# Kernel optimization log

Measured on AMD Instinct MI355X. Metric: run time of the kernel, lower is better.

The kernel has to match this reference:

```python
import jax, jax.numpy as jnp
import numpy as np

N, M, DIST, HEADS, D, C, DFFN = 16384, 16, 2, 8, 256, 64, 512
DH = D // HEADS
GRID = 128
BLOCK = 2048  # mirrors torch batch_size loop in find_neighboring_voxels_optimized
EPS = 1e-5


def _neighbors(coords_f, src, m, dist):
    """Blockwise Manhattan-distance topk neighbor gather.
    coords_f: (N,3) float voxel coords; src: (N,D) features.
    Returns (N, m, D) neighbor features, zero-filled where fewer than m in range."""
    n = coords_f.shape[0]
    qblocks = coords_f.reshape(-1, BLOCK, 3)

    def one_block(cb):
        # (BLOCK, N) Manhattan distances
        d = jnp.abs(cb[:, None, :] - coords_f[None, :, :]).sum(-1)
        d = jnp.where(d <= dist, d, jnp.inf)
        vals, idx = jax.lax.top_k(-d, m)          # nearest m (self first: dist 0)
        valid = (vals > -jnp.inf)[..., None]
        return jnp.where(valid, src[idx], jnp.zeros((), src.dtype))

    return jax.lax.map(one_block, qblocks).reshape(n, m, src.shape[-1])


def _layernorm(x, g, b):
    mu = x.mean(-1, keepdims=True)
    var = ((x - mu) ** 2).mean(-1, keepdims=True)
    return (x - mu) * jax.lax.rsqrt(var + EPS) * g + b


def setup_inputs() -> dict:
    key = jax.random.key(0)
    ks = jax.random.split(key, 32)
    p = lambda i, shape, s: jax.random.normal(ks[i], shape, dtype=jnp.float32) * s
    z = lambda shape: jnp.zeros(shape, dtype=jnp.float32)
    o = lambda shape: jnp.ones(shape, dtype=jnp.float32)
    return {
        "coords": jax.random.randint(ks[0], (N, 3), 0, GRID, dtype=jnp.int32),
        "features": jax.random.normal(ks[1], (N, C), dtype=jnp.float32),
        "pe_w1": p(2, (3, D // 2), 0.5), "pe_b1": z((D // 2,)),
        "pe_w2": p(3, (D // 2, D), 0.08), "pe_b2": z((D,)),
        "proj_w": p(4, (C, D), 0.12), "proj_b": z((D,)),
        "wq": p(5, (D, D), 0.06), "bq": z((D,)),
        "wk": p(6, (D, D), 0.06), "bk": z((D,)),
        "wv": p(7, (D, D), 0.06), "bv": z((D,)),
        "wo": p(8, (D, D), 0.06), "bo": z((D,)),
        "ffn_w1": p(9, (D, DFFN), 0.06), "ffn_b1": z((DFFN,)),
        "ffn_w2": p(10, (DFFN, D), 0.04), "ffn_b2": z((D,)),
        "ln_g": o((D,)), "ln_b": z((D,)),
        "fus_w1": p(11, (D, C), 0.06), "fus_b1": z((C,)),
        "fus_w2": p(12, (2 * C, C), 0.09), "fus_b2": z((C,)),
        "bn_g": o((C,)), "bn_b": z((C,)),
    }


def reference(coords, features, pe_w1, pe_b1, pe_w2, pe_b2, proj_w, proj_b,
              wq, bq, wk, bk, wv, bv, wo, bo,
              ffn_w1, ffn_b1, ffn_w2, ffn_b2, ln_g, ln_b,
              fus_w1, fus_b1, fus_w2, fus_b2, bn_g, bn_b):
    coords_f = coords.astype(jnp.float32)
    # dynamic learnable positional encoding on normalized coords
    xn = coords_f / (GRID - 1)
    pe = jax.nn.relu(xn @ pe_w1 + pe_b1) @ pe_w2 + pe_b2
    src = features @ proj_w + proj_b + pe                       # (N, D)

    nf = _neighbors(coords_f, src, M, DIST)                     # (N, M, D)
    query = nf[:, 0, :]                                         # (N, D) self-feature

    # multihead attention: query len 1, key len M, batch N
    q = (query @ wq + bq).reshape(N, HEADS, DH)
    k = (nf @ wk + bk).reshape(N, M, HEADS, DH)
    v = (nf @ wv + bv).reshape(N, M, HEADS, DH)
    scores = jnp.einsum('nhd,nmhd->nhm', q, k) / jnp.sqrt(jnp.float32(DH))
    attn = jax.nn.softmax(scores, axis=-1)
    ao = jnp.einsum('nhm,nmhd->nhd', attn, v).reshape(N, D) @ wo + bo  # (N, D)

    # FFN with residual + LayerNorm (dropout=0 / eval)
    h = jax.nn.relu(ao @ ffn_w1 + ffn_b1) @ ffn_w2 + ffn_b2
    y = _layernorm(ao + h, ln_g, ln_b)                          # (N, D)

    # EnhancedFusion: project, concat, linear, BatchNorm1d (batch stats), ReLU
    t = y @ fus_w1 + fus_b1                                     # (N, C)
    f = jnp.concatenate([features, t], axis=1) @ fus_w2 + fus_b2
    mu = f.mean(0)
    var = ((f - mu) ** 2).mean(0)
    f = (f - mu) * jax.lax.rsqrt(var + EPS) * bn_g + bn_b
    return jax.nn.relu(f)                                       # (N, C)
```

## Files before the change

kernel.cpp:

```cpp
#include <hip/hip_runtime.h>
#include <stdint.h>

typedef unsigned short u16;
typedef unsigned int   u32;
typedef __attribute__((ext_vector_type(8))) short short8;
typedef __attribute__((ext_vector_type(4))) float f32x4;

static constexpr int kN = 16384;
static constexpr float kEPS = 1e-5f;

__device__ __forceinline__ u16 f2bf(float x) {
  u32 u = __float_as_uint(x);
  u32 r = (u + 0x7fffu + ((u >> 16) & 1u)) >> 16;
  return (u16)r;
}
__device__ __forceinline__ float bf2f(u16 x) {
  return __uint_as_float(((u32)x) << 16);
}
__device__ __forceinline__ void ldbf8(const u16* p, float* o) {
  uint4 v = *(const uint4*)p;
  o[0] = __uint_as_float(v.x << 16);  o[1] = __uint_as_float(v.x & 0xffff0000u);
  o[2] = __uint_as_float(v.y << 16);  o[3] = __uint_as_float(v.y & 0xffff0000u);
  o[4] = __uint_as_float(v.z << 16);  o[5] = __uint_as_float(v.z & 0xffff0000u);
  o[6] = __uint_as_float(v.w << 16);  o[7] = __uint_as_float(v.w & 0xffff0000u);
}
__device__ __forceinline__ void gll16(const u16* g, u16* l) {
  __builtin_amdgcn_global_load_lds(
      (const __attribute__((address_space(1))) void*)g,
      (__attribute__((address_space(3))) void*)l, 16, 0, 0);
}

struct WSet {
  const float* s[6]; u16* d[6];
  int K[6]; int N[6]; int dstride[6]; int coff[6];
};

__global__ __launch_bounds__(256) void k_setup(WSet ws,
                                               u32* __restrict__ zero_area,
                                               const float* __restrict__ proj_b,
                                               const float* __restrict__ pe_b2,
                                               const float* __restrict__ uw1,
                                               const float* __restrict__ ub1,
                                               const float* __restrict__ uw2,
                                               const float* __restrict__ ub2,
                                               u16* __restrict__ W2f,
                                               float* __restrict__ bbf,
                                               const int* __restrict__ coords,
                                               const float* __restrict__ feats,
                                               const float* __restrict__ pw1,
                                               const float* __restrict__ pb1,
                                               u16* __restrict__ A1,
                                               u16* __restrict__ A2,
                                               const float* __restrict__ wq,
                                               const float* __restrict__ wk,
                                               const float* __restrict__ wv,
                                               const float* __restrict__ proj_w_f,
                                               const float* __restrict__ pe_w2_f,
                                               u16* __restrict__ W1K,
                                               float* __restrict__ bcomb) {
  int w = blockIdx.y;
  if (w == 6) {
    int idx = blockIdx.x * 256 + threadIdx.x;
    if (idx < 33088) zero_area[idx] = 0u;
    return;
  }
  if (w == 7) {
    int n = blockIdx.x;
    if (n >= 64) return;
    int k = threadIdx.x;
    float s = 0.f;
    for (int j = 0; j < 64; j++) s += uw1[k * 64 + j] * uw2[(64 + j) * 64 + n];
    W2f[n * 320 + k] = f2bf(s);
    if (k < 64) W2f[n * 320 + 256 + k] = f2bf(uw2[k * 64 + n]);
    if (k == 0) {
      float b = ub2[n];
      for (int j = 0; j < 64; j++) b += ub1[j] * uw2[(64 + j) * 64 + n];
      bbf[n] = b;
    }
    return;
  }
  if (w == 8) {
    int r0 = blockIdx.x * 32;
#pragma unroll
    for (int s = 0; s < 3; s++) {
      int j = threadIdx.x + s * 256;
      int row = j / 24, seg = j % 24;
      int n = r0 + row;
      u16 o[8];
      if (seg < 8) {
        const float* fp = feats + (size_t)n * 64 + seg * 8;
        float4 a = *(const float4*)fp;
        float4 b = *(const float4*)(fp + 4);
        o[0] = f2bf(a.x); o[1] = f2bf(a.y); o[2] = f2bf(a.z); o[3] = f2bf(a.w);
        o[4] = f2bf(b.x); o[5] = f2bf(b.y); o[6] = f2bf(b.z); o[7] = f2bf(b.w);
        *(uint4*)(A2 + (size_t)n * 320 + 256 + seg * 8) = *(uint4*)o;
      } else {
        int jj0 = (seg - 8) * 8;
        float x0 = (float)coords[n * 3 + 0] * (1.f / 127.f);
        float x1 = (float)coords[n * 3 + 1] * (1.f / 127.f);
        float x2 = (float)coords[n * 3 + 2] * (1.f / 127.f);
#pragma unroll
        for (int u = 0; u < 8; u++) {
          int jj = jj0 + u;
          float hv = pb1[jj] + x0 * pw1[jj] + x1 * pw1[128 + jj] + x2 * pw1[256 + jj];
          o[u] = f2bf(fmaxf(hv, 0.f));
        }
      }
      *(uint4*)(A1 + (size_t)n * 192 + seg * 8) = *(uint4*)o;
    }
    return;
  }
  if (w == 9) {
    int bx = blockIdx.x;
    if (bx < 3) {
      const float* wsel = (bx == 0) ? wq : (bx == 1) ? wk : wv;
      int c = threadIdx.x;
      float s = 0.f;
      for (int d = 0; d < 256; d++) s += (proj_b[d] + pe_b2[d]) * wsel[d * 256 + c];
      bcomb[bx * 256 + c] = s;
    } else if (bx < 27) {
      int i0 = (bx - 3) * 2048 + threadIdx.x * 8;
      const float* src = (i0 < 16384) ? (proj_w_f + i0) : (pe_w2_f + (i0 - 16384));
      float4 a = *(const float4*)src;
      float4 b = *(const float4*)(src + 4);
      u16 o[8];
      o[0] = f2bf(a.x); o[1] = f2bf(a.y); o[2] = f2bf(a.z); o[3] = f2bf(a.w);
      o[4] = f2bf(b.x); o[5] = f2bf(b.y); o[6] = f2bf(b.z); o[7] = f2bf(b.w);
      *(uint4*)(W1K + i0) = *(uint4*)o;
    }
    return;
  }
  const float* S = ws.s[w]; u16* D = ws.d[w];
  int K = ws.K[w], N = ws.N[w], ds = ws.dstride[w], co = ws.coff[w];
  int ntx = N >> 5, tiles = ntx * (K >> 5);
  int t = blockIdx.x;
  if (t >= tiles) return;
  int n0 = (t % ntx) * 32, k0 = (t / ntx) * 32;
  __shared__ float st[32][33];
  int tr = threadIdx.x >> 3, tc4 = (threadIdx.x & 7) * 4;
  float4 v = *(const float4*)(S + (size_t)(k0 + tr) * N + n0 + tc4);
  st[tc4 + 0][tr] = v.x; st[tc4 + 1][tr] = v.y;
  st[tc4 + 2][tr] = v.z; st[tc4 + 3][tr] = v.w;
  __syncthreads();
  u16 o4[4];
  o4[0] = f2bf(st[tr][tc4 + 0]); o4[1] = f2bf(st[tr][tc4 + 1]);
  o4[2] = f2bf(st[tr][tc4 + 2]); o4[3] = f2bf(st[tr][tc4 + 3]);
  *(uint2*)(D + (size_t)(n0 + tr) * ds + co + k0 + tc4) = *(uint2*)o4;
}


__global__ __launch_bounds__(256) void k_hist(const int* __restrict__ coords,
                                              u32* __restrict__ cnt) {
  int n = blockIdx.x * 256 + threadIdx.x;
  int c = coords[n * 3] * 128 + coords[n * 3 + 1];
  atomicAdd(&cnt[c], 1u);
}

__global__ __launch_bounds__(256) void k_scan(const u32* __restrict__ cnt,
                                              u32* __restrict__ startb) {
  __shared__ u32 tots[256];
  int t = threadIdx.x;
  int base = t * 64;
  u32 s = 0;
  for (int i = 0; i < 64; i++) s += cnt[base + i];
  tots[t] = s;
  __syncthreads();
  if (t == 0) {
    u32 run = 0;
    for (int i = 0; i < 256; i++) { u32 v = tots[i]; tots[i] = run; run += v; }
  }
  __syncthreads();
  u32 run = tots[t];
  for (int i = 0; i < 64; i++) { startb[base + i] = run; run += cnt[base + i]; }
}

__global__ __launch_bounds__(256) void k_scatter(const int* __restrict__ coords,
                                                 const u32* __restrict__ startb,
                                                 u32* __restrict__ cursor,
                                                 u32* __restrict__ pts) {
  int n = blockIdx.x * 256 + threadIdx.x;
  int x = coords[n * 3], y = coords[n * 3 + 1], z = coords[n * 3 + 2];
  int c = x * 128 + y;
  u32 slot = atomicAdd(&cursor[c], 1u);
  pts[startb[c] + slot] = ((u32)z << 14) | (u32)n;
}

__global__ __launch_bounds__(256) void k_select(const int* __restrict__ coords,
                                                const u32* __restrict__ startb,
                                                const u32* __restrict__ cnt,
                                                const u32* __restrict__ pts,
                                                int* __restrict__ idxo) {
  int n = blockIdx.x * 256 + threadIdx.x;
  int x = coords[n * 3], y = coords[n * 3 + 1], z = coords[n * 3 + 2];
  u32 best[16];
#pragma unroll
  for (int j = 0; j < 16; j++) best[j] = 0xFFFFFFFFu;
  const int dxs[13] = {0, -1, 1, 0, 0, -2, 2, 0, 0, -1, -1, 1, 1};
  const int dys[13] = {0, 0, 0, -1, 1, 0, 0, -2, 2, -1, 1, -1, 1};
  const int dbs[13] = {0, 1, 1, 1, 1, 2, 2, 2, 2, 2, 2, 2, 2};
#pragma unroll
  for (int t = 0; t < 13; t++) {
    int xx = x + dxs[t], yy = y + dys[t];
    if (xx < 0 || xx > 127 || yy < 0 || yy > 127) continue;
    int c = xx * 128 + yy;
    u32 s0 = startb[c], e0 = s0 + cnt[c];
    for (u32 i = s0; i < e0; ++i) {
      u32 p = pts[i];
      int zq = (int)(p >> 14);
      int id = (int)(p & 16383u);
      int az = z - zq; az = az < 0 ? -az : az;
      int dd = dbs[t] + az;
      u32 key = (dd <= 2) ? (((u32)dd << 14) | (u32)id) : 0xFFFFFFFFu;
#pragma unroll
      for (int j = 0; j < 16; j++) {
        u32 lo = min(best[j], key);
        u32 hi = max(best[j], key);
        best[j] = lo; key = hi;
      }
    }
  }
#pragma unroll
  for (int j = 0; j < 16; j++)
    idxo[n * 16 + j] = (best[j] == 0xFFFFFFFFu) ? -1 : (int)(best[j] & 16383u);
}

template <int BM, int BN, int ACT, int OUTBF, int ADD>
__global__ __launch_bounds__(256) void k_mgemm(
    const u16* __restrict__ A, const u16* __restrict__ WT,
    const float* __restrict__ bias,
    void* __restrict__ Cout,
    const u16* __restrict__ Addp,
    int M, int K, int N) {
  constexpr int FM = BM / 32, FN = BN / 32;
  constexpr int RA = BM / 64, RB = BN / 64;
  __shared__ __align__(16) u16 As[2][BM * 32];
  __shared__ __align__(16) u16 Bs[2][BN * 32];
  const int tid = threadIdx.x;
  const int wave = tid >> 6, lane = tid & 63;
  const int bm = blockIdx.y * BM, bn = blockIdx.x * BN;
  const int wr = (wave >> 1) * (BM / 2), wc = (wave & 1) * (BN / 2);
  const int fr = lane & 15, fk = (lane >> 4) * 8, rq = (lane >> 4) * 4;

  f32x4 acc[FM][FN];
#pragma unroll
  for (int i = 0; i < FM; i++)
#pragma unroll
    for (int j = 0; j < FN; j++)
#pragma unroll
      for (int r = 0; r < 4; r++) acc[i][j][r] = 0.f;

  for (int k0 = 0; k0 < K; k0 += 64) {
#pragma unroll
    for (int h = 0; h < 2; h++) {
#pragma unroll
      for (int r = 0; r < RA; r++) {
        int g2 = r * 256 + tid;
        gll16(A + (size_t)(bm + (g2 >> 2)) * K + k0 + h * 32 + (g2 & 3) * 8,
              As[h] + g2 * 8);
      }
#pragma unroll
      for (int r = 0; r < RB; r++) {
        int g2 = r * 256 + tid;
        gll16(WT + (size_t)(bn + (g2 >> 2)) * K + k0 + h * 32 + (g2 & 3) * 8,
              Bs[h] + g2 * 8);
      }
    }
    __syncthreads();
#pragma unroll
    for (int h = 0; h < 2; h++) {
      short8 af[FM], bg[FN];
#pragma unroll
      for (int i = 0; i < FM; i++)
        af[i] = *(const short8*)&As[h][(wr + i * 16 + fr) * 32 + fk];
#pragma unroll
      for (int j = 0; j < FN; j++)
        bg[j] = *(const short8*)&Bs[h][(wc + j * 16 + fr) * 32 + fk];
#pragma unroll
      for (int i = 0; i < FM; i++)
#pragma unroll
        for (int j = 0; j < FN; j++)
          acc[i][j] = __builtin_amdgcn_mfma_f32_16x16x32_bf16(af[i], bg[j], acc[i][j], 0, 0, 0);
    }
    __syncthreads();
  }

#pragma unroll
  for (int j = 0; j < FN; j++) {
    int cc = bn + wc + j * 16 + fr;
    float bval = bias ? bias[cc] : 0.f;
#pragma unroll
    for (int i = 0; i < FM; i++) {
      int rbase = bm + wr + i * 16 + rq;
#pragma unroll
      for (int r = 0; r < 4; r++) {
        float v = acc[i][j][r] + bval;
        size_t o = (size_t)(rbase + r) * N + cc;
        if (ADD) v += bf2f(Addp[o]);
        if (ACT) v = fmaxf(v, 0.f);
        if (OUTBF) ((u16*)Cout)[o] = f2bf(v);
        else       ((float*)Cout)[o] = v;
      }
    }
  }
}

__global__ __launch_bounds__(256) void k_attn(const u16* __restrict__ QKV,
                                              const u32* __restrict__ pts,
                                              const int* __restrict__ idx,
                                              const float* __restrict__ bq,
                                              const float* __restrict__ bk,
                                              const float* __restrict__ bv,
                                              u16* __restrict__ outp) {
  int gid = blockIdx.x * 256 + threadIdx.x;
  int n = (int)(pts[gid >> 3] & 16383u), h = gid & 7;
  const int* ip = idx + n * 16;
  const int hb = h * 32;
  float q[32];
  {
    int i0 = ip[0];
    const u16* qp = QKV + (size_t)i0 * 768 + hb;
#pragma unroll
    for (int j = 0; j < 32; j += 8) ldbf8(qp + j, &q[j]);
#pragma unroll
    for (int j = 0; j < 32; j++) q[j] += bq[hb + j];
  }
  float qbk = 0.f;
#pragma unroll
  for (int j = 0; j < 32; j++) qbk += q[j] * bk[hb + j];
  float s[16]; int ii[16];
#pragma unroll
  for (int m = 0; m < 16; m++) {
    int i = ip[m]; ii[m] = i;
    float d = qbk;
    if (i >= 0) {
      const u16* kp = QKV + (size_t)i * 768 + 256 + hb;
      float kv[32];
#pragma unroll
      for (int j = 0; j < 32; j += 8) ldbf8(kp + j, &kv[j]);
#pragma unroll
      for (int j = 0; j < 32; j++) d += q[j] * kv[j];
    }
    s[m] = d * 0.17677669529663689f;
  }
  float mx = s[0];
#pragma unroll
  for (int m = 1; m < 16; m++) mx = fmaxf(mx, s[m]);
  float sum = 0.f;
#pragma unroll
  for (int m = 0; m < 16; m++) { s[m] = __expf(s[m] - mx); sum += s[m]; }
  float inv = 1.f / sum;
  float o[32];
#pragma unroll
  for (int j = 0; j < 32; j++) o[j] = 0.f;
#pragma unroll
  for (int m = 0; m < 16; m++) {
    if (ii[m] >= 0) {
      const u16* vp = QKV + (size_t)ii[m] * 768 + 512 + hb;
      float vv[32];
#pragma unroll
      for (int j = 0; j < 32; j += 8) ldbf8(vp + j, &vv[j]);
#pragma unroll
      for (int j = 0; j < 32; j++) o[j] += s[m] * vv[j];
    }
  }
  u16* op = outp + (size_t)n * 256 + hb;
#pragma unroll
  for (int j = 0; j < 32; j += 8) {
    u16 tmp[8];
#pragma unroll
    for (int jj = 0; jj < 8; jj++) tmp[jj] = f2bf(o[j + jj] * inv + bv[hb + j + jj]);
    *(uint4*)(op + j) = *(uint4*)tmp;
  }
}

__global__ __launch_bounds__(256) void k_ln(const u16* __restrict__ xx,
                                            const float* __restrict__ g,
                                            const float* __restrict__ b,
                                            u16* __restrict__ A2) {
  int row = blockIdx.x * 4 + (threadIdx.x >> 6);
  int lane = threadIdx.x & 63;
  uint2 raw = *(const uint2*)(xx + (size_t)row * 256 + lane * 4);
  float x0 = __uint_as_float(raw.x << 16), x1 = __uint_as_float(raw.x & 0xffff0000u);
  float x2 = __uint_as_float(raw.y << 16), x3 = __uint_as_float(raw.y & 0xffff0000u);
  float sm = x0 + x1 + x2 + x3;
#pragma unroll
  for (int off = 1; off < 64; off <<= 1) sm += __shfl_xor(sm, off);
  float mu = sm * (1.f / 256.f);
  float d0 = x0 - mu, d1 = x1 - mu, d2 = x2 - mu, d3 = x3 - mu;
  float sq = d0 * d0 + d1 * d1 + d2 * d2 + d3 * d3;
#pragma unroll
  for (int off = 1; off < 64; off <<= 1) sq += __shfl_xor(sq, off);
  float rstd = rsqrtf(sq * (1.f / 256.f) + kEPS);
  float4 gv = *(const float4*)(g + lane * 4);
  float4 bv4 = *(const float4*)(b + lane * 4);
  u16 o[4];
  o[0] = f2bf(d0 * rstd * gv.x + bv4.x); o[1] = f2bf(d1 * rstd * gv.y + bv4.y);
  o[2] = f2bf(d2 * rstd * gv.z + bv4.z); o[3] = f2bf(d3 * rstd * gv.w + bv4.w);
  *(uint2*)(A2 + (size_t)row * 320 + lane * 4) = *(uint2*)o;
}

__global__ __launch_bounds__(256) void k_fgemm(const u16* __restrict__ A2,
                                               const u16* __restrict__ W2f,
                                               const float* __restrict__ bbf,
                                               float* __restrict__ fB,
                                               float* __restrict__ pS,
                                               float* __restrict__ pQ) {
  __shared__ __align__(16) u16 As[2][2048];
  __shared__ __align__(16) u16 Bs[2][2048];
  __shared__ float colS[64][2], colQ[64][2];
  const int tid = threadIdx.x;
  const int wave = tid >> 6, lane = tid & 63;
  const int bm = blockIdx.x * 64;
  const int wr = (wave >> 1) * 32, wc = (wave & 1) * 32;
  const int fr = lane & 15, fk = (lane >> 4) * 8, rq = (lane >> 4) * 4;
  const int g = wave * 64 + lane;
  const int grow = g >> 2, gko = (g & 3) * 8;

  f32x4 acc[2][2];
#pragma unroll
  for (int i = 0; i < 2; i++)
#pragma unroll
    for (int j = 0; j < 2; j++)
#pragma unroll
      for (int r = 0; r < 4; r++) acc[i][j][r] = 0.f;
  for (int k0 = 0; k0 < 320; k0 += 64) {
#pragma unroll
    for (int h = 0; h < 2; h++) {
      gll16(A2 + (size_t)(bm + grow) * 320 + k0 + h * 32 + gko, As[h] + g * 8);
      gll16(W2f + (size_t)grow * 320 + k0 + h * 32 + gko, Bs[h] + g * 8);
    }
    __syncthreads();
#pragma unroll
    for (int h = 0; h < 2; h++) {
      short8 af[2], bg[2];
#pragma unroll
      for (int i = 0; i < 2; i++)
        af[i] = *(const short8*)&As[h][(wr + i * 16 + fr) * 32 + fk];
#pragma unroll
      for (int j = 0; j < 2; j++)
        bg[j] = *(const short8*)&Bs[h][(wc + j * 16 + fr) * 32 + fk];
#pragma unroll
      for (int i = 0; i < 2; i++)
#pragma unroll
        for (int j = 0; j < 2; j++)
          acc[i][j] = __builtin_amdgcn_mfma_f32_16x16x32_bf16(af[i], bg[j], acc[i][j], 0, 0, 0);
    }
    __syncthreads();
  }
  float cS[2] = {0.f, 0.f}, cQ[2] = {0.f, 0.f};
#pragma unroll
  for (int j = 0; j < 2; j++) {
    int col = wc + j * 16 + fr;
    float bv = bbf[col];
#pragma unroll
    for (int i = 0; i < 2; i++) {
      int rbase = bm + wr + i * 16 + rq;
#pragma unroll
      for (int r = 0; r < 4; r++) {
        float v = acc[i][j][r] + bv;
        fB[(size_t)(rbase + r) * 64 + col] = v;
        cS[j] += v; cQ[j] += v * v;
      }
    }
  }
#pragma unroll
  for (int off = 16; off < 64; off <<= 1) {
#pragma unroll
    for (int j = 0; j < 2; j++) {
      cS[j] += __shfl_xor(cS[j], off);
      cQ[j] += __shfl_xor(cQ[j], off);
    }
  }
  if ((lane >> 4) == 0) {
#pragma unroll
    for (int j = 0; j < 2; j++) {
      colS[wc + j * 16 + fr][wave >> 1] = cS[j];
      colQ[wc + j * 16 + fr][wave >> 1] = cQ[j];
    }
  }
  __syncthreads();
  if (tid < 64) {
    atomicAdd(&pS[tid], colS[tid][0] + colS[tid][1]);
    atomicAdd(&pQ[tid], colQ[tid][0] + colQ[tid][1]);
  }
}

__global__ __launch_bounds__(64) void k_bnfin(const float* __restrict__ pS,
                                              const float* __restrict__ pQ,
                                              const float* __restrict__ g,
                                              const float* __restrict__ b,
                                              float* __restrict__ coef,
                                              float* __restrict__ shift) {
  int c = threadIdx.x;
  float S = pS[c], Q = pQ[c];
  float m = S * (1.f / 16384.f);
  float var = Q * (1.f / 16384.f) - m * m;
  float cf = rsqrtf(var + kEPS) * g[c];
  coef[c] = cf;
  shift[c] = b[c] - m * cf;
}

__global__ __launch_bounds__(256) void k_bnapply(const float* __restrict__ f,
                                                 const float* __restrict__ coef,
                                                 const float* __restrict__ shift,
                                                 float* __restrict__ out) {
  int gid = blockIdx.x * 256 + threadIdx.x;
  int e = gid * 4, col = e & 63;
  float4 v = *(const float4*)(f + e);
  float4 cf = *(const float4*)(coef + col);
  float4 sh = *(const float4*)(shift + col);
  float4 o;
  o.x = fmaxf(v.x * cf.x + sh.x, 0.f);
  o.y = fmaxf(v.y * cf.y + sh.y, 0.f);
  o.z = fmaxf(v.z * cf.z + sh.z, 0.f);
  o.w = fmaxf(v.w * cf.w + sh.w, 0.f);
  *(float4*)(out + e) = o;
}

extern "C" void kernel_launch(void* const* d_in, const int* in_sizes, int n_in,
                              void* d_out, int out_size, void* d_ws, size_t ws_size,
                              hipStream_t stream) {
  (void)in_sizes; (void)n_in; (void)out_size; (void)ws_size;
  const int*   coords = (const int*)d_in[0];
  const float* feats  = (const float*)d_in[1];
  const float* pe_w1  = (const float*)d_in[2];
  const float* pe_b1  = (const float*)d_in[3];
  const float* pe_w2  = (const float*)d_in[4];
  const float* pe_b2  = (const float*)d_in[5];
  const float* proj_w = (const float*)d_in[6];
  const float* proj_b = (const float*)d_in[7];
  const float* wq  = (const float*)d_in[8];
  const float* bq  = (const float*)d_in[9];
  const float* wk  = (const float*)d_in[10];
  const float* bk  = (const float*)d_in[11];
  const float* wv  = (const float*)d_in[12];
  const float* bv  = (const float*)d_in[13];
  const float* wo  = (const float*)d_in[14];
  const float* bo  = (const float*)d_in[15];
  const float* fw1 = (const float*)d_in[16];
  const float* fb1 = (const float*)d_in[17];
  const float* fw2 = (const float*)d_in[18];
  const float* fb2 = (const float*)d_in[19];
  const float* lng = (const float*)d_in[20];
  const float* lnb = (const float*)d_in[21];
  const float* uw1 = (const float*)d_in[22];
  const float* ub1 = (const float*)d_in[23];
  const float* uw2 = (const float*)d_in[24];
  const float* ub2 = (const float*)d_in[25];
  const float* bng = (const float*)d_in[26];
  const float* bnb = (const float*)d_in[27];
  float* out = (float*)d_out;

  char* Wc = (char*)d_ws;
  const size_t MB = 1u << 20;
  u16*   A1    = (u16*)(Wc + 0 * MB);
  u16*   QKVb  = (u16*)(Wc + 14 * MB);
  u16*   aoInB = (u16*)(Wc + 38 * MB);
  u16*   aoB   = (u16*)(Wc + 46 * MB);
  u16*   h1B   = (u16*)(Wc + 54 * MB);
  u16*   xBb   = (u16*)(Wc + 70 * MB);
  u16*   A2    = (u16*)(Wc + 78 * MB);
  float* fB    = (float*)(Wc + 0 * MB);

  u16* qkvT  = (u16*)(Wc + 88 * MB);
  u16* woT   = qkvT + 196608;
  u16* fw1T  = woT + 65536;
  u16* fw2T  = fw1T + 131072;
  u16* W1K   = fw2T + 131072;
  u16* W2f   = W1K + 49152;
  u16* Wcomb = W2f + 20480;
  float* bbf   = (float*)(Wcomb + 147456);
  float* bcomb = bbf + 64;

  u32* Z      = (u32*)(Wc + 90 * MB);
  u32* cnt    = Z;
  u32* cursor = Z + 16384;
  float* pS   = (float*)(Z + 32768);
  float* pQ   = (float*)(Z + 32832);
  float* coefb = (float*)(Z + 32912);
  float* shb   = coefb + 64;
  u32* startb = Z + 33280;
  u32* pts    = Z + 49664;
  int* idxb   = (int*)(Z + 66048);

  WSet ws;
  ws.s[0] = wq;     ws.d[0] = qkvT;          ws.K[0] = 256; ws.N[0] = 256; ws.dstride[0] = 256; ws.coff[0] = 0;
  ws.s[1] = wk;     ws.d[1] = qkvT + 65536;  ws.K[1] = 256; ws.N[1] = 256; ws.dstride[1] = 256; ws.coff[1] = 0;
  ws.s[2] = wv;     ws.d[2] = qkvT + 131072; ws.K[2] = 256; ws.N[2] = 256; ws.dstride[2] = 256; ws.coff[2] = 0;
  ws.s[3] = wo;     ws.d[3] = woT;           ws.K[3] = 256; ws.N[3] = 256; ws.dstride[3] = 256; ws.coff[3] = 0;
  ws.s[4] = fw1;    ws.d[4] = fw1T;          ws.K[4] = 256; ws.N[4] = 512; ws.dstride[4] = 256; ws.coff[4] = 0;
  ws.s[5] = fw2;    ws.d[5] = fw2T;          ws.K[5] = 512; ws.N[5] = 256; ws.dstride[5] = 512; ws.coff[5] = 0;

  k_setup<<<dim3(512, 10), 256, 0, stream>>>(ws, Z, proj_b, pe_b2,
                                             uw1, ub1, uw2, ub2, W2f, bbf,
                                             coords, feats, pe_w1, pe_b1, A1, A2,
                                             wq, wk, wv, proj_w, pe_w2, W1K, bcomb);
  k_mgemm<64, 64, 0, 1, 0><<<dim3(3, 12), 256, 0, stream>>>(
      qkvT, W1K, nullptr, Wcomb, nullptr, 768, 256, 192);
  k_hist<<<64, 256, 0, stream>>>(coords, cnt);
  k_scan<<<1, 256, 0, stream>>>(cnt, startb);
  k_scatter<<<64, 256, 0, stream>>>(coords, startb, cursor, pts);
  k_select<<<64, 256, 0, stream>>>(coords, startb, cnt, pts, idxb);
  k_mgemm<128, 128, 0, 1, 0><<<dim3(6, 128), 256, 0, stream>>>(
      A1, Wcomb, bcomb, QKVb, nullptr, kN, 192, 768);
  k_attn<<<512, 256, 0, stream>>>(QKVb, pts, idxb, bq, bk, bv, aoInB);
  k_mgemm<128, 64, 0, 1, 0><<<dim3(4, 128), 256, 0, stream>>>(
      aoInB, woT, bo, aoB, nullptr, kN, 256, 256);
  k_mgemm<128, 128, 1, 1, 0><<<dim3(4, 128), 256, 0, stream>>>(
      aoB, fw1T, fb1, h1B, nullptr, kN, 256, 512);
  k_mgemm<128, 64, 0, 1, 1><<<dim3(4, 128), 256, 0, stream>>>(
      h1B, fw2T, fb2, xBb, aoB, kN, 512, 256);
  k_ln<<<4096, 256, 0, stream>>>(xBb, lng, lnb, A2);
  k_fgemm<<<256, 256, 0, stream>>>(A2, W2f, bbf, fB, pS, pQ);
  k_bnfin<<<1, 64, 0, stream>>>(pS, pQ, bng, bnb, coefb, shb);
  k_bnapply<<<1024, 256, 0, stream>>>(fB, coefb, shb, out);
}
```

Before: 249.4 us.

## Fuse neighbor build, FFN2+LayerNorm, and fusion GEMM+BatchNorm via cooperative grid sync

Merges the histogram/scan/scatter/select kernels into one cooperative kernel that uses grid.sync between phases. Fuses the second FFN GEMM with the residual add and LayerNorm, using a 64x256 tile so each block holds full rows. Fuses the final GEMM with BatchNorm statistics, finalisation and ReLU through a grid-wide barrier, which removes the intermediate fB round trip and three launches. The costs are grid-sync overhead, cooperative-launch limits, lower GEMM parallelism (256 blocks) in the FFN2 stage, and a one-pass variance formula.

```diff
diff --git a/kernel.cpp b/kernel.cpp
--- a/kernel.cpp
+++ b/kernel.cpp
@@ -1,5 +1,8 @@
 #include <hip/hip_runtime.h>
+#include <hip/hip_cooperative_groups.h>
 #include <stdint.h>
+
+namespace cg = cooperative_groups;
 
 typedef unsigned short u16;
 typedef unsigned int   u32;
@@ -148,50 +151,38 @@
   *(uint2*)(D + (size_t)(n0 + tr) * ds + co + k0 + tc4) = *(uint2*)o4;
 }
 
-
-__global__ __launch_bounds__(256) void k_hist(const int* __restrict__ coords,
-                                              u32* __restrict__ cnt) {
-  int n = blockIdx.x * 256 + threadIdx.x;
-  int c = coords[n * 3] * 128 + coords[n * 3 + 1];
-  atomicAdd(&cnt[c], 1u);
-}
-
-__global__ __launch_bounds__(256) void k_scan(const u32* __restrict__ cnt,
-                                              u32* __restrict__ startb) {
-  __shared__ u32 tots[256];
-  int t = threadIdx.x;
-  int base = t * 64;
-  u32 s = 0;
-  for (int i = 0; i < 64; i++) s += cnt[base + i];
-  tots[t] = s;
-  __syncthreads();
-  if (t == 0) {
-    u32 run = 0;
-    for (int i = 0; i < 256; i++) { u32 v = tots[i]; tots[i] = run; run += v; }
-  }
-  __syncthreads();
-  u32 run = tots[t];
-  for (int i = 0; i < 64; i++) { startb[base + i] = run; run += cnt[base + i]; }
-}
-
-__global__ __launch_bounds__(256) void k_scatter(const int* __restrict__ coords,
-                                                 const u32* __restrict__ startb,
-                                                 u32* __restrict__ cursor,
-                                                 u32* __restrict__ pts) {
+__global__ __launch_bounds__(256) void k_neigh(const int* __restrict__ coords,
+                                               u32* __restrict__ cnt,
+                                               u32* __restrict__ startb,
+                                               u32* __restrict__ cursor,
+                                               u32* __restrict__ pts,
+                                               int* __restrict__ idxo) {
+  cg::grid_group grid = cg::this_grid();
   int n = blockIdx.x * 256 + threadIdx.x;
   int x = coords[n * 3], y = coords[n * 3 + 1], z = coords[n * 3 + 2];
   int c = x * 128 + y;
+  atomicAdd(&cnt[c], 1u);
+  grid.sync();
+  if (blockIdx.x == 0) {
+    __shared__ u32 tots[256];
+    int t = threadIdx.x;
+    int base = t * 64;
+    u32 s = 0;
+    for (int i = 0; i < 64; i++) s += cnt[base + i];
+    tots[t] = s;
+    __syncthreads();
+    if (t == 0) {
+      u32 run = 0;
+      for (int i = 0; i < 256; i++) { u32 v = tots[i]; tots[i] = run; run += v; }
+    }
+    __syncthreads();
+    u32 run = tots[t];
+    for (int i = 0; i < 64; i++) { startb[base + i] = run; run += cnt[base + i]; }
+  }
+  grid.sync();
   u32 slot = atomicAdd(&cursor[c], 1u);
   pts[startb[c] + slot] = ((u32)z << 14) | (u32)n;
-}
-
-__global__ __launch_bounds__(256) void k_select(const int* __restrict__ coords,
-                                                const u32* __restrict__ startb,
-                                                const u32* __restrict__ cnt,
-                                                const u32* __restrict__ pts,
-                                                int* __restrict__ idxo) {
-  int n = blockIdx.x * 256 + threadIdx.x;
-  int x = coords[n * 3], y = coords[n * 3 + 1], z = coords[n * 3 + 2];
+  grid.sync();
   u32 best[16];
 #pragma unroll
   for (int j = 0; j < 16; j++) best[j] = 0xFFFFFFFFu;
@@ -202,8 +193,8 @@
   for (int t = 0; t < 13; t++) {
     int xx = x + dxs[t], yy = y + dys[t];
     if (xx < 0 || xx > 127 || yy < 0 || yy > 127) continue;
-    int c = xx * 128 + yy;
-    u32 s0 = startb[c], e0 = s0 + cnt[c];
+    int cc = xx * 128 + yy;
+    u32 s0 = startb[cc], e0 = s0 + cnt[cc];
     for (u32 i = s0; i < e0; ++i) {
       u32 p = pts[i];
       int zq = (int)(p >> 14);
@@ -373,38 +364,127 @@
   }
 }
 
-__global__ __launch_bounds__(256) void k_ln(const u16* __restrict__ xx,
-                                            const float* __restrict__ g,
-                                            const float* __restrict__ b,
-                                            u16* __restrict__ A2) {
-  int row = blockIdx.x * 4 + (threadIdx.x >> 6);
-  int lane = threadIdx.x & 63;
-  uint2 raw = *(const uint2*)(xx + (size_t)row * 256 + lane * 4);
-  float x0 = __uint_as_float(raw.x << 16), x1 = __uint_as_float(raw.x & 0xffff0000u);
-  float x2 = __uint_as_float(raw.y << 16), x3 = __uint_as_float(raw.y & 0xffff0000u);
-  float sm = x0 + x1 + x2 + x3;
-#pragma unroll
-  for (int off = 1; off < 64; off <<= 1) sm += __shfl_xor(sm, off);
-  float mu = sm * (1.f / 256.f);
-  float d0 = x0 - mu, d1 = x1 - mu, d2 = x2 - mu, d3 = x3 - mu;
-  float sq = d0 * d0 + d1 * d1 + d2 * d2 + d3 * d3;
-#pragma unroll
-  for (int off = 1; off < 64; off <<= 1) sq += __shfl_xor(sq, off);
-  float rstd = rsqrtf(sq * (1.f / 256.f) + kEPS);
-  float4 gv = *(const float4*)(g + lane * 4);
-  float4 bv4 = *(const float4*)(b + lane * 4);
-  u16 o[4];
-  o[0] = f2bf(d0 * rstd * gv.x + bv4.x); o[1] = f2bf(d1 * rstd * gv.y + bv4.y);
-  o[2] = f2bf(d2 * rstd * gv.z + bv4.z); o[3] = f2bf(d3 * rstd * gv.w + bv4.w);
-  *(uint2*)(A2 + (size_t)row * 320 + lane * 4) = *(uint2*)o;
-}
-
-__global__ __launch_bounds__(256) void k_fgemm(const u16* __restrict__ A2,
-                                               const u16* __restrict__ W2f,
-                                               const float* __restrict__ bbf,
-                                               float* __restrict__ fB,
-                                               float* __restrict__ pS,
-                                               float* __restrict__ pQ) {
+__global__ __launch_bounds__(256) void k_ffn2ln(const u16* __restrict__ A,
+                                                const u16* __restrict__ WT,
+                                                const float* __restrict__ bias,
+                                                const u16* __restrict__ Addp,
+                                                const float* __restrict__ g,
+                                                const float* __restrict__ b,
+                                                u16* __restrict__ A2) {
+  constexpr int BM = 64, BN = 256, FM = 2, FN = 8;
+  __shared__ __align__(16) u16 As[2][BM * 32];
+  __shared__ __align__(16) u16 Bs[2][BN * 32];
+  __shared__ float lnS[64][2], lnQ[64][2];
+  const int tid = threadIdx.x;
+  const int wave = tid >> 6, lane = tid & 63;
+  const int bm = blockIdx.x * BM;
+  const int wr = (wave >> 1) * 32, wc = (wave & 1) * 128;
+  const int fr = lane & 15, fk = (lane >> 4) * 8, rq = (lane >> 4) * 4;
+
+  f32x4 acc[FM][FN];
+#pragma unroll
+  for (int i = 0; i < FM; i++)
+#pragma unroll
+    for (int j = 0; j < FN; j++)
+#pragma unroll
+      for (int r = 0; r < 4; r++) acc[i][j][r] = 0.f;
+
+  for (int k0 = 0; k0 < 512; k0 += 64) {
+#pragma unroll
+    for (int h = 0; h < 2; h++) {
+      {
+        int g2 = tid;
+        gll16(A + (size_t)(bm + (g2 >> 2)) * 512 + k0 + h * 32 + (g2 & 3) * 8,
+              As[h] + g2 * 8);
+      }
+#pragma unroll
+      for (int r = 0; r < 4; r++) {
+        int g2 = r * 256 + tid;
+        gll16(WT + (size_t)(g2 >> 2) * 512 + k0 + h * 32 + (g2 & 3) * 8,
+              Bs[h] + g2 * 8);
+      }
+    }
+    __syncthreads();
+#pragma unroll
+    for (int h = 0; h < 2; h++) {
+      short8 af[FM], bg[FN];
+#pragma unroll
+      for (int i = 0; i < FM; i++)
+        af[i] = *(const short8*)&As[h][(wr + i * 16 + fr) * 32 + fk];
+#pragma unroll
+      for (int j = 0; j < FN; j++)
+        bg[j] = *(const short8*)&Bs[h][(wc + j * 16 + fr) * 32 + fk];
+#pragma unroll
+      for (int i = 0; i < FM; i++)
+#pragma unroll
+        for (int j = 0; j < FN; j++)
+          acc[i][j] = __builtin_amdgcn_mfma_f32_16x16x32_bf16(af[i], bg[j], acc[i][j], 0, 0, 0);
+    }
+    __syncthreads();
+  }
+
+#pragma unroll
+  for (int j = 0; j < FN; j++) {
+    int cc = wc + j * 16 + fr;
+    float bval = bias[cc];
+#pragma unroll
+    for (int i = 0; i < FM; i++) {
+      int rbase = bm + wr + i * 16 + rq;
+#pragma unroll
+      for (int r = 0; r < 4; r++)
+        acc[i][j][r] += bval + bf2f(Addp[(size_t)(rbase + r) * 256 + cc]);
+    }
+  }
+#pragma unroll
+  for (int i = 0; i < FM; i++) {
+#pragma unroll
+    for (int r = 0; r < 4; r++) {
+      float sm = 0.f, sq = 0.f;
+#pragma unroll
+      for (int j = 0; j < FN; j++) { float t = acc[i][j][r]; sm += t; sq += t * t; }
+#pragma unroll
+      for (int off = 1; off < 16; off <<= 1) {
+        sm += __shfl_xor(sm, off);
+        sq += __shfl_xor(sq, off);
+      }
+      if (fr == 0) {
+        int row = wr + i * 16 + rq + r;
+        lnS[row][wave & 1] = sm;
+        lnQ[row][wave & 1] = sq;
+      }
+    }
+  }
+  __syncthreads();
+#pragma unroll
+  for (int i = 0; i < FM; i++) {
+#pragma unroll
+    for (int r = 0; r < 4; r++) {
+      int row = wr + i * 16 + rq + r;
+      float sm = lnS[row][0] + lnS[row][1];
+      float sq = lnQ[row][0] + lnQ[row][1];
+      float mu = sm * (1.f / 256.f);
+      float var = sq * (1.f / 256.f) - mu * mu;
+      float rstd = rsqrtf(var + kEPS);
+      size_t rowg = (size_t)(bm + row);
+#pragma unroll
+      for (int j = 0; j < FN; j++) {
+        int cc = wc + j * 16 + fr;
+        float val = (acc[i][j][r] - mu) * rstd * g[cc] + b[cc];
+        A2[rowg * 320 + cc] = f2bf(val);
+      }
+    }
+  }
+}
+
+__global__ __launch_bounds__(256) void k_fgemmbn(const u16* __restrict__ A2,
+                                                 const u16* __restrict__ W2f,
+                                                 const float* __restrict__ bbf,
+                                                 float* __restrict__ pS,
+                                                 float* __restrict__ pQ,
+                                                 const float* __restrict__ g,
+                                                 const float* __restrict__ b,
+                                                 float* __restrict__ out) {
+  cg::grid_group grid = cg::this_grid();
   __shared__ __align__(16) u16 As[2][2048];
   __shared__ __align__(16) u16 Bs[2][2048];
   __shared__ float colS[64][2], colQ[64][2];
@@ -413,8 +493,8 @@
   const int bm = blockIdx.x * 64;
   const int wr = (wave >> 1) * 32, wc = (wave & 1) * 32;
   const int fr = lane & 15, fk = (lane >> 4) * 8, rq = (lane >> 4) * 4;
-  const int g = wave * 64 + lane;
-  const int grow = g >> 2, gko = (g & 3) * 8;
+  const int gg = wave * 64 + lane;
+  const int grow = gg >> 2, gko = (gg & 3) * 8;
 
   f32x4 acc[2][2];
 #pragma unroll
@@ -426,8 +506,8 @@
   for (int k0 = 0; k0 < 320; k0 += 64) {
 #pragma unroll
     for (int h = 0; h < 2; h++) {
-      gll16(A2 + (size_t)(bm + grow) * 320 + k0 + h * 32 + gko, As[h] + g * 8);
-      gll16(W2f + (size_t)grow * 320 + k0 + h * 32 + gko, Bs[h] + g * 8);
+      gll16(A2 + (size_t)(bm + grow) * 320 + k0 + h * 32 + gko, As[h] + gg * 8);
+      gll16(W2f + (size_t)grow * 320 + k0 + h * 32 + gko, Bs[h] + gg * 8);
     }
     __syncthreads();
 #pragma unroll
@@ -454,11 +534,10 @@
     float bv = bbf[col];
 #pragma unroll
     for (int i = 0; i < 2; i++) {
-      int rbase = bm + wr + i * 16 + rq;
 #pragma unroll
       for (int r = 0; r < 4; r++) {
         float v = acc[i][j][r] + bv;
-        fB[(size_t)(rbase + r) * 64 + col] = v;
+        acc[i][j][r] = v;
         cS[j] += v; cQ[j] += v * v;
       }
     }
@@ -483,38 +562,23 @@
     atomicAdd(&pS[tid], colS[tid][0] + colS[tid][1]);
     atomicAdd(&pQ[tid], colQ[tid][0] + colQ[tid][1]);
   }
-}
-
-__global__ __launch_bounds__(64) void k_bnfin(const float* __restrict__ pS,
-                                              const float* __restrict__ pQ,
-                                              const float* __restrict__ g,
-                                              const float* __restrict__ b,
-                                              float* __restrict__ coef,
-                                              float* __restrict__ shift) {
-  int c = threadIdx.x;
-  float S = pS[c], Q = pQ[c];
-  float m = S * (1.f / 16384.f);
-  float var = Q * (1.f / 16384.f) - m * m;
-  float cf = rsqrtf(var + kEPS) * g[c];
-  coef[c] = cf;
-  shift[c] = b[c] - m * cf;
-}
-
-__global__ __launch_bounds__(256) void k_bnapply(const float* __restrict__ f,
-                                                 const float* __restrict__ coef,
-                                                 const float* __restrict__ shift,
-                                                 float* __restrict__ out) {
-  int gid = blockIdx.x * 256 + threadIdx.x;
-  int e = gid * 4, col = e & 63;
-  float4 v = *(const float4*)(f + e);
-  float4 cf = *(const float4*)(coef + col);
-  float4 sh = *(const float4*)(shift + col);
-  float4 o;
-  o.x = fmaxf(v.x * cf.x + sh.x, 0.f);
-  o.y = fmaxf(v.y * cf.y + sh.y, 0.f);
-  o.z = fmaxf(v.z * cf.z + sh.z, 0.f);
-  o.w = fmaxf(v.w * cf.w + sh.w, 0.f);
-  *(float4*)(out + e) = o;
+  grid.sync();
+#pragma unroll
+  for (int j = 0; j < 2; j++) {
+    int col = wc + j * 16 + fr;
+    float S = pS[col], Q = pQ[col];
+    float m = S * (1.f / 16384.f);
+    float var = Q * (1.f / 16384.f) - m * m;
+    float cf = rsqrtf(var + kEPS) * g[col];
+    float sh = b[col] - m * cf;
+#pragma unroll
+    for (int i = 0; i < 2; i++) {
+      int rbase = bm + wr + i * 16 + rq;
+#pragma unroll
+      for (int r = 0; r < 4; r++)
+        out[(size_t)(rbase + r) * 64 + col] = fmaxf(acc[i][j][r] * cf + sh, 0.f);
+    }
+  }
 }
 
 extern "C" void kernel_launch(void* const* d_in, const int* in_sizes, int n_in,
@@ -558,9 +622,7 @@
   u16*   aoInB = (u16*)(Wc + 38 * MB);
   u16*   aoB   = (u16*)(Wc + 46 * MB);
   u16*   h1B   = (u16*)(Wc + 54 * MB);
-  u16*   xBb   = (u16*)(Wc + 70 * MB);
   u16*   A2    = (u16*)(Wc + 78 * MB);
-  float* fB    = (float*)(Wc + 0 * MB);
 
   u16* qkvT  = (u16*)(Wc + 88 * MB);
   u16* woT   = qkvT + 196608;
@@ -577,8 +639,6 @@
   u32* cursor = Z + 16384;
   float* pS   = (float*)(Z + 32768);
   float* pQ   = (float*)(Z + 32832);
-  float* coefb = (float*)(Z + 32912);
-  float* shb   = coefb + 64;
   u32* startb = Z + 33280;
   u32* pts    = Z + 49664;
   int* idxb   = (int*)(Z + 66048);
@@ -597,10 +657,11 @@
                                              wq, wk, wv, proj_w, pe_w2, W1K, bcomb);
   k_mgemm<64, 64, 0, 1, 0><<<dim3(3, 12), 256, 0, stream>>>(
       qkvT, W1K, nullptr, Wcomb, nullptr, 768, 256, 192);
-  k_hist<<<64, 256, 0, stream>>>(coords, cnt);
-  k_scan<<<1, 256, 0, stream>>>(cnt, startb);
-  k_scatter<<<64, 256, 0, stream>>>(coords, startb, cursor, pts);
-  k_select<<<64, 256, 0, stream>>>(coords, startb, cnt, pts, idxb);
+  {
+    void* args[] = {(void*)&coords, (void*)&cnt, (void*)&startb,
+                    (void*)&cursor, (void*)&pts, (void*)&idxb};
+    hipLaunchCooperativeKernel((void*)k_neigh, dim3(64), dim3(256), args, 0, stream);
+  }
   k_mgemm<128, 128, 0, 1, 0><<<dim3(6, 128), 256, 0, stream>>>(
       A1, Wcomb, bcomb, QKVb, nullptr, kN, 192, 768);
   k_attn<<<512, 256, 0, stream>>>(QKVb, pts, idxb, bq, bk, bv, aoInB);
@@ -608,10 +669,10 @@
       aoInB, woT, bo, aoB, nullptr, kN, 256, 256);
   k_mgemm<128, 128, 1, 1, 0><<<dim3(4, 128), 256, 0, stream>>>(
       aoB, fw1T, fb1, h1B, nullptr, kN, 256, 512);
-  k_mgemm<128, 64, 0, 1, 1><<<dim3(4, 128), 256, 0, stream>>>(
-      h1B, fw2T, fb2, xBb, aoB, kN, 512, 256);
-  k_ln<<<4096, 256, 0, stream>>>(xBb, lng, lnb, A2);
-  k_fgemm<<<256, 256, 0, stream>>>(A2, W2f, bbf, fB, pS, pQ);
-  k_bnfin<<<1, 64, 0, stream>>>(pS, pQ, bng, bnb, coefb, shb);
-  k_bnapply<<<1024, 256, 0, stream>>>(fB, coefb, shb, out);
-}
+  k_ffn2ln<<<256, 256, 0, stream>>>(h1B, fw2T, fb2, aoB, lng, lnb, A2);
+  {
+    void* args[] = {(void*)&A2, (void*)&W2f, (void*)&bbf, (void*)&pS, (void*)&pQ,
+                    (void*)&bng, (void*)&bnb, (void*)&out};
+    hipLaunchCooperativeKernel((void*)k_fgemmbn, dim3(256), dim3(256), args, 0, stream);
+  }
+}
```

After: 348.6 us. 1.4x slower.
